# Kernel tuning notes

Hardware: AMD Instinct MI355X
Metric: run time of the kernel (lower is better)

The kernel has to match this reference:

```python
import jax, jax.numpy as jnp
import numpy as np

B, CH, XL, YL = 512, 1, 64, 64
H = 64                       # num_heads
D = CH * XL * YL             # 4096
F = D // H                   # feature_dim = 64 (== H, required by the mask multiply)


def setup_inputs() -> dict:
    key = jax.random.key(0)
    k1, k2, k3, k4, k5 = jax.random.split(key, 5)
    scale = 1.0 / np.sqrt(D)  # roughly kaiming-ish init for square linears
    return {
        "x": jax.random.normal(k1, (B, CH, XL, YL), dtype=jnp.float32),
        "interface_map": jax.random.uniform(k2, (B, CH, XL, YL), dtype=jnp.float32),
        "Wq": jax.random.normal(k3, (D, D), dtype=jnp.float32) * scale,
        "Wk": jax.random.normal(k4, (D, D), dtype=jnp.float32) * scale,
        "Wv": jax.random.normal(k5, (D, D), dtype=jnp.float32) * scale,
    }


def reference(x, interface_map, Wq, Wk, Wv):
    b = x.shape[0]
    xf = x.reshape(b, D)
    # nn.Linear(bias=False): y = x @ W.T
    q = (xf @ Wq.T).reshape(b, H, F)
    k = (xf @ Wk.T).reshape(b, H, F)
    v = (xf @ Wv.T).reshape(b, H, F)
    inv_sqrt_f = jnp.float32(1.0 / np.sqrt(F))
    qk_t = jnp.einsum("bhf,bgf->bhg", q, k) * inv_sqrt_f           # (B, H, H)
    qk_t = qk_t * interface_map.reshape(b, H, F)                   # multiplicative mask (F == H)
    attention_weights = jax.nn.softmax(qk_t, axis=-1)
    weighted_values = jnp.einsum("bhg,bgf->bhf", attention_weights, v)  # (B, H, F)
    combined = jnp.swapaxes(weighted_values, 1, 2).reshape(b, CH, XL, YL)
    output = x * combined
    return output, attention_weights
```

## Files before the change

kernel.cpp:

```cpp
#include <hip/hip_runtime.h>
#include <cstdint>
#include <cstddef>

typedef __attribute__((ext_vector_type(8))) short short8;
typedef __attribute__((ext_vector_type(4))) float f32x4;

#define NB 512
#define DD 4096
#define NP 12288

__device__ __forceinline__ unsigned pk2(float a, float b) {
    unsigned r;
    asm("v_cvt_pk_bf16_f32 %0, %1, %2" : "=v"(r) : "v"(a), "v"(b));
    return r;
}

__device__ __forceinline__ void gload_lds16(const void* g, void* l) {
    __builtin_amdgcn_global_load_lds((const __attribute__((address_space(1))) void*)g,
                                     (__attribute__((address_space(3))) void*)l, 16, 0, 0);
}

__global__ __launch_bounds__(256) void cvt_bf16_kernel(const float* __restrict__ src,
                                                       unsigned short* __restrict__ dst,
                                                       int n8) {
    int i = blockIdx.x * 256 + threadIdx.x;
    if (i >= n8) return;
    const float4* s = (const float4*)src + (size_t)i * 2;
    float4 a = s[0], b = s[1];
    uint4 r;
    r.x = pk2(a.x, a.y);
    r.y = pk2(a.z, a.w);
    r.z = pk2(b.x, b.y);
    r.w = pk2(b.z, b.w);
    ((uint4*)dst)[i] = r;
}

template<int KS>
__global__ __launch_bounds__(256, 3) void gemm_qkv_kernel(
    const unsigned short* __restrict__ xb,
    const float* __restrict__ w0, const float* __restrict__ w1, const float* __restrict__ w2,
    float* __restrict__ part)
{
    constexpr int KLEN = DD / KS;
    constexpr int NIT = KLEN / 32;
    constexpr int NWG = 96 * 4 * KS;
    constexpr int CPX = NWG / 8;

    const int bid = blockIdx.x;
    const int orig = (bid & 7) * CPX + (bid >> 3);
    const int nt = orig / (4 * KS);
    const int rest = orig - nt * (4 * KS);
    const int mt = rest / KS;
    const int kz = rest - mt * KS;

    const float* W = (nt < 32) ? w0 : ((nt < 64) ? w1 : w2);
    const int ntl = nt & 31;
    const float* Wbase = W + (size_t)(ntl * 128) * DD + kz * KLEN;
    const unsigned short* Abase = xb + (size_t)(mt * 128) * DD + kz * KLEN;
    float* C = part + (size_t)kz * NB * NP;

    __shared__ unsigned short As[4][128 * 32];
    __shared__ unsigned short Bs[2][128 * 32];

    const int t = threadIdx.x;
    const int l = t & 63;
    const int wv = t >> 6;
    const int wr = wv >> 1, wc = wv & 1;

    f32x4 acc[4][4];
    #pragma unroll
    for (int i = 0; i < 4; ++i)
        #pragma unroll
        for (int j = 0; j < 4; ++j)
            acc[i][j] = (f32x4){0.f, 0.f, 0.f, 0.f};

    const int arow0 = (t >> 2);
    const int acol  = (((t & 3) ^ ((t >> 3) & 3)) * 8);

    const int brow0 = t >> 3;
    const int bc8   = t & 7;
    const float* wsrc = Wbase + (size_t)brow0 * DD + bc8 * 4;
    char* bwp[4];
    #pragma unroll
    for (int p = 0; p < 4; ++p) {
        int r = p * 32 + brow0;
        bwp[p] = (char*)(&Bs[0][0]) + r * 64 + (((bc8 >> 1) ^ ((r >> 1) & 3)) * 16) + (bc8 & 1) * 8;
    }
    const int cx = ((l >> 4) ^ ((l >> 1) & 3));

    float4 bregA[4], bregB[4];

    #define LOADB(br, kt)  { _Pragma("unroll") for (int p = 0; p < 4; ++p) \
                               br[p] = *(const float4*)(wsrc + (size_t)(p * 32) * DD + (kt) * 32); }
    #define STAGEA(kt, buf) { _Pragma("unroll") for (int i = 0; i < 2; ++i) \
                               gload_lds16(Abase + (size_t)(i * 64 + arow0) * DD + (kt) * 32 + acol, \
                                           (char*)(&As[buf][0]) + i * 4096 + wv * 1024); }
    #define WRITEB(br, buf) { _Pragma("unroll") for (int p = 0; p < 4; ++p) { \
                                uint2 q; \
                                q.x = pk2(br[p].x, br[p].y); \
                                q.y = pk2(br[p].z, br[p].w); \
                                *(uint2*)(bwp[p] + (buf) * 8192) = q; } }
    #define BAR() { asm volatile("s_waitcnt lgkmcnt(0)" ::: "memory"); \
                    __builtin_amdgcn_s_barrier(); }

    STAGEA(0, 0);
    LOADB(bregA, 0);
    STAGEA(1, 1);
    WRITEB(bregA, 0);
    LOADB(bregB, 1);
    BAR();

    #define ITER(kt, ac, ap, bc, bn, bwr, bld) { \
        if ((kt) + 2 < NIT) { STAGEA((kt) + 2, ap); LOADB(bld, (kt) + 2); } \
        short8 af[4], bfr[4]; \
        _Pragma("unroll") for (int fi = 0; fi < 4; ++fi) { \
            int row = wr * 64 + fi * 16 + (l & 15); \
            af[fi] = *(const short8*)((const char*)(&As[ac][0]) + row * 64 + cx * 16); \
        } \
        _Pragma("unroll") for (int fj = 0; fj < 4; ++fj) { \
            int row = wc * 64 + fj * 16 + (l & 15); \
            bfr[fj] = *(const short8*)((const char*)(&Bs[bc][0]) + row * 64 + cx * 16); \
        } \
        _Pragma("unroll") for (int fi = 0; fi < 4; ++fi) \
            _Pragma("unroll") for (int fj = 0; fj < 4; ++fj) \
                acc[fi][fj] = __builtin_amdgcn_mfma_f32_16x16x32_bf16(af[fi], bfr[fj], acc[fi][fj], 0, 0, 0); \
        if ((kt) + 1 < NIT) WRITEB(bwr, bn); \
        BAR(); \
    }

    for (int kt = 0; kt < NIT; kt += 4) {
        ITER(kt + 0, 0, 2, 0, 1, bregB, bregA);
        ITER(kt + 1, 1, 3, 1, 0, bregA, bregB);
        ITER(kt + 2, 2, 0, 0, 1, bregB, bregA);
        ITER(kt + 3, 3, 1, 1, 0, bregA, bregB);
    }
    #undef ITER
    #undef LOADB
    #undef STAGEA
    #undef WRITEB
    #undef BAR

    #pragma unroll
    for (int fi = 0; fi < 4; ++fi) {
        int rbase = mt * 128 + wr * 64 + fi * 16 + (l >> 4) * 4;
        #pragma unroll
        for (int fj = 0; fj < 4; ++fj) {
            int col = nt * 128 + wc * 64 + fj * 16 + (l & 15);
            #pragma unroll
            for (int r = 0; r < 4; ++r)
                C[(size_t)(rbase + r) * NP + col] = acc[fi][fj][r];
        }
    }
}

template<int KS>
__global__ __launch_bounds__(256) void attn_kernel(
    const float* __restrict__ part,
    const float* __restrict__ x,
    const float* __restrict__ imap,
    float* __restrict__ dout)
{
    const int b = blockIdx.x;
    const int t = threadIdx.x;
    const int l = t & 63;
    const int wv = t >> 6;

    __shared__ float sq[64 * 68];
    __shared__ float sk[64 * 68];
    __shared__ float sv[64 * 68];

    const float* base0 = part + (size_t)b * NP;
    const float* base1 = part + (size_t)NB * NP + (size_t)b * NP;

    #pragma unroll
    for (int i = 0; i < 4; ++i) {
        int f4 = i * 256 + t;
        int r = f4 >> 4, c = (f4 & 15) * 4;
        float4 q4 = *(const float4*)(base0 + (size_t)f4 * 4);
        float4 k4 = *(const float4*)(base0 + DD + (size_t)f4 * 4);
        float4 v4 = *(const float4*)(base0 + 2 * DD + (size_t)f4 * 4);
        if (KS == 2) {
            float4 a4 = *(const float4*)(base1 + (size_t)f4 * 4);
            float4 b4 = *(const float4*)(base1 + DD + (size_t)f4 * 4);
            float4 c4 = *(const float4*)(base1 + 2 * DD + (size_t)f4 * 4);
            q4.x += a4.x; q4.y += a4.y; q4.z += a4.z; q4.w += a4.w;
            k4.x += b4.x; k4.y += b4.y; k4.z += b4.z; k4.w += b4.w;
            v4.x += c4.x; v4.y += c4.y; v4.z += c4.z; v4.w += c4.w;
        }
        *(float4*)(&sq[r * 68 + c]) = q4;
        *(float4*)(&sk[r * 68 + c]) = k4;
        *(float4*)(&sv[r * 68 + c]) = v4;
    }
    __syncthreads();

    float accs[16];
    #pragma unroll
    for (int i = 0; i < 16; ++i) accs[i] = 0.f;
    #pragma unroll 4
    for (int f4 = 0; f4 < 16; ++f4) {
        float4 kvv = *(const float4*)(&sk[l * 68 + f4 * 4]);
        #pragma unroll
        for (int i = 0; i < 16; ++i) {
            int h = i * 4 + wv;
            float4 qv = *(const float4*)(&sq[h * 68 + f4 * 4]);
            accs[i] = fmaf(qv.x, kvv.x, fmaf(qv.y, kvv.y, fmaf(qv.z, kvv.z, fmaf(qv.w, kvv.w, accs[i]))));
        }
    }
    __syncthreads();
    #pragma unroll
    for (int i = 0; i < 16; ++i) {
        int h = i * 4 + wv;
        float m = imap[(size_t)b * DD + h * 64 + l];
        sk[h * 65 + l] = accs[i] * 0.125f * m;
    }
    __syncthreads();

    {
        int h = t >> 2, j = t & 3;
        float e[16];
        float mx = -3.0e38f;
        #pragma unroll
        for (int q2 = 0; q2 < 16; ++q2) {
            e[q2] = sk[h * 65 + j * 16 + q2];
            mx = fmaxf(mx, e[q2]);
        }
        mx = fmaxf(mx, __shfl_xor(mx, 1));
        mx = fmaxf(mx, __shfl_xor(mx, 2));
        float s = 0.f;
        #pragma unroll
        for (int q2 = 0; q2 < 16; ++q2) { e[q2] = __expf(e[q2] - mx); s += e[q2]; }
        s += __shfl_xor(s, 1);
        s += __shfl_xor(s, 2);
        float invs = 1.0f / s;
        float* aw = dout + (size_t)NB * DD + (size_t)b * DD + h * 64 + j * 16;
        #pragma unroll
        for (int q2 = 0; q2 < 16; q2 += 4) {
            float4 w4 = {e[q2] * invs, e[q2 + 1] * invs, e[q2 + 2] * invs, e[q2 + 3] * invs};
            *(float4*)(aw + q2) = w4;
            sk[h * 65 + j * 16 + q2 + 0] = w4.x;
            sk[h * 65 + j * 16 + q2 + 1] = w4.y;
            sk[h * 65 + j * 16 + q2 + 2] = w4.z;
            sk[h * 65 + j * 16 + q2 + 3] = w4.w;
        }
    }
    __syncthreads();

    float pacc[16];
    #pragma unroll
    for (int i = 0; i < 16; ++i) pacc[i] = 0.f;
    #pragma unroll 4
    for (int g = 0; g < 64; ++g) {
        float p = sk[l * 65 + g];
        const float4* vr = (const float4*)(&sv[g * 68 + wv * 16]);
        float4 v0 = vr[0], v1 = vr[1], v2 = vr[2], v3 = vr[3];
        pacc[0]  = fmaf(p, v0.x, pacc[0]);
        pacc[1]  = fmaf(p, v0.y, pacc[1]);
        pacc[2]  = fmaf(p, v0.z, pacc[2]);
        pacc[3]  = fmaf(p, v0.w, pacc[3]);
        pacc[4]  = fmaf(p, v1.x, pacc[4]);
        pacc[5]  = fmaf(p, v1.y, pacc[5]);
        pacc[6]  = fmaf(p, v1.z, pacc[6]);
        pacc[7]  = fmaf(p, v1.w, pacc[7]);
        pacc[8]  = fmaf(p, v2.x, pacc[8]);
        pacc[9]  = fmaf(p, v2.y, pacc[9]);
        pacc[10] = fmaf(p, v2.z, pacc[10]);
        pacc[11] = fmaf(p, v2.w, pacc[11]);
        pacc[12] = fmaf(p, v3.x, pacc[12]);
        pacc[13] = fmaf(p, v3.y, pacc[13]);
        pacc[14] = fmaf(p, v3.z, pacc[14]);
        pacc[15] = fmaf(p, v3.w, pacc[15]);
    }
    const size_t ob = (size_t)b * DD + (size_t)(wv * 16) * 64 + l;
    #pragma unroll
    for (int ii = 0; ii < 16; ++ii) {
        size_t o = ob + (size_t)ii * 64;
        dout[o] = x[o] * pacc[ii];
    }
}

extern "C" void kernel_launch(void* const* d_in, const int* in_sizes, int n_in,
                              void* d_out, int out_size, void* d_ws, size_t ws_size,
                              hipStream_t stream) {
    const float* x  = (const float*)d_in[0];
    const float* im = (const float*)d_in[1];
    const float* Wq = (const float*)d_in[2];
    const float* Wk = (const float*)d_in[3];
    const float* Wv = (const float*)d_in[4];
    float* out = (float*)d_out;

    unsigned short* xb = (unsigned short*)d_ws;
    float* part = (float*)((char*)d_ws + (size_t)NB * DD * 2);

    const size_t need2 = (size_t)NB * DD * 2 + 2ull * NB * NP * 4;
    const int KS = (ws_size >= need2) ? 2 : 1;

    cvt_bf16_kernel<<<dim3((NB * DD / 8 + 255) / 256), dim3(256), 0, stream>>>(x, xb, NB * DD / 8);

    if (KS == 2) {
        gemm_qkv_kernel<2><<<dim3(96 * 4 * 2), dim3(256), 0, stream>>>(xb, Wq, Wk, Wv, part);
        attn_kernel<2><<<dim3(NB), dim3(256), 0, stream>>>(part, x, im, out);
    } else {
        gemm_qkv_kernel<1><<<dim3(96 * 4 * 1), dim3(256), 0, stream>>>(xb, Wq, Wk, Wv, part);
        attn_kernel<1><<<dim3(NB), dim3(256), 0, stream>>>(part, x, im, out);
    }
}
```

Before: 129.1 us.

## Deepen QKV GEMM prefetch pipeline to three stages with MFMA priority boost

The QKV projection GEMM now prefetches A tiles and B register tiles three iterations ahead instead of two. It rotates three B register sets and unrolls by 12 so buffer indices stay compile-time constants. MFMA blocks are wrapped in s_setprio to favour the compute wave, and the main loop barriers only wait on LDS counters, with a full vmcnt wait kept for the tail iterations. The aim is to hide more global load latency, at the cost of more registers, which could cut occupancy under launch_bounds(256,3), and a fragile loop-trip computation.

```diff
diff --git a/kernel.cpp b/kernel.cpp
--- a/kernel.cpp
+++ b/kernel.cpp
@@ -43,6 +43,7 @@
 {
     constexpr int KLEN = DD / KS;
     constexpr int NIT = KLEN / 32;
+    constexpr int KMAIN = ((NIT - 4) / 12) * 12;
     constexpr int NWG = 96 * 4 * KS;
     constexpr int CPX = NWG / 8;
 
@@ -88,7 +89,7 @@
     }
     const int cx = ((l >> 4) ^ ((l >> 1) & 3));
 
-    float4 bregA[4], bregB[4];
+    float4 b0[4], b1[4], b2[4];
 
     #define LOADB(br, kt)  { _Pragma("unroll") for (int p = 0; p < 4; ++p) \
                                br[p] = *(const float4*)(wsrc + (size_t)(p * 32) * DD + (kt) * 32); }
@@ -100,45 +101,82 @@
                                 q.x = pk2(br[p].x, br[p].y); \
                                 q.y = pk2(br[p].z, br[p].w); \
                                 *(uint2*)(bwp[p] + (buf) * 8192) = q; } }
-    #define BAR() { asm volatile("s_waitcnt lgkmcnt(0)" ::: "memory"); \
-                    __builtin_amdgcn_s_barrier(); }
-
-    STAGEA(0, 0);
-    LOADB(bregA, 0);
-    STAGEA(1, 1);
-    WRITEB(bregA, 0);
-    LOADB(bregB, 1);
-    BAR();
-
-    #define ITER(kt, ac, ap, bc, bn, bwr, bld) { \
-        if ((kt) + 2 < NIT) { STAGEA((kt) + 2, ap); LOADB(bld, (kt) + 2); } \
+    #define BARL() { asm volatile("s_waitcnt lgkmcnt(0)" ::: "memory"); \
+                     __builtin_amdgcn_s_barrier(); }
+    #define BARF() { asm volatile("s_waitcnt vmcnt(0) lgkmcnt(0)" ::: "memory"); \
+                     __builtin_amdgcn_s_barrier(); }
+
+    #define COMPUTE(abuf, bbuf) { \
         short8 af[4], bfr[4]; \
         _Pragma("unroll") for (int fi = 0; fi < 4; ++fi) { \
             int row = wr * 64 + fi * 16 + (l & 15); \
-            af[fi] = *(const short8*)((const char*)(&As[ac][0]) + row * 64 + cx * 16); \
+            af[fi] = *(const short8*)((const char*)(&As[abuf][0]) + row * 64 + cx * 16); \
         } \
         _Pragma("unroll") for (int fj = 0; fj < 4; ++fj) { \
             int row = wc * 64 + fj * 16 + (l & 15); \
-            bfr[fj] = *(const short8*)((const char*)(&Bs[bc][0]) + row * 64 + cx * 16); \
+            bfr[fj] = *(const short8*)((const char*)(&Bs[bbuf][0]) + row * 64 + cx * 16); \
         } \
+        __builtin_amdgcn_s_setprio(1); \
         _Pragma("unroll") for (int fi = 0; fi < 4; ++fi) \
             _Pragma("unroll") for (int fj = 0; fj < 4; ++fj) \
                 acc[fi][fj] = __builtin_amdgcn_mfma_f32_16x16x32_bf16(af[fi], bfr[fj], acc[fi][fj], 0, 0, 0); \
-        if ((kt) + 1 < NIT) WRITEB(bwr, bn); \
-        BAR(); \
-    }
-
-    for (int kt = 0; kt < NIT; kt += 4) {
-        ITER(kt + 0, 0, 2, 0, 1, bregB, bregA);
-        ITER(kt + 1, 1, 3, 1, 0, bregA, bregB);
-        ITER(kt + 2, 2, 0, 0, 1, bregB, bregA);
-        ITER(kt + 3, 3, 1, 1, 0, bregA, bregB);
-    }
-    #undef ITER
+        __builtin_amdgcn_s_setprio(0); \
+    }
+
+    #define ITER_M(kt, s, bl, bw) { \
+        STAGEA((kt) + 3, ((s) + 3) & 3); \
+        LOADB(bl, (kt) + 3); \
+        COMPUTE((s) & 3, (s) & 1); \
+        WRITEB(bw, ((s) + 1) & 1); \
+        BARL(); }
+
+    #define ITER_T(kt, s, bl, bw) { \
+        if ((kt) < NIT) { \
+            if ((kt) + 3 < NIT) { STAGEA((kt) + 3, ((s) + 3) & 3); LOADB(bl, (kt) + 3); } \
+            COMPUTE((s) & 3, (s) & 1); \
+            if ((kt) + 1 < NIT) WRITEB(bw, ((s) + 1) & 1); \
+            BARF(); } }
+
+    STAGEA(0, 0);
+    STAGEA(1, 1);
+    STAGEA(2, 2);
+    LOADB(b0, 0);
+    LOADB(b1, 1);
+    LOADB(b2, 2);
+    WRITEB(b0, 0);
+    BARL();
+
+    for (int kt0 = 0; kt0 < KMAIN; kt0 += 12) {
+        ITER_M(kt0 + 0,  0,  b0, b1);
+        ITER_M(kt0 + 1,  1,  b1, b2);
+        ITER_M(kt0 + 2,  2,  b2, b0);
+        ITER_M(kt0 + 3,  3,  b0, b1);
+        ITER_M(kt0 + 4,  4,  b1, b2);
+        ITER_M(kt0 + 5,  5,  b2, b0);
+        ITER_M(kt0 + 6,  6,  b0, b1);
+        ITER_M(kt0 + 7,  7,  b1, b2);
+        ITER_M(kt0 + 8,  8,  b2, b0);
+        ITER_M(kt0 + 9,  9,  b0, b1);
+        ITER_M(kt0 + 10, 10, b1, b2);
+        ITER_M(kt0 + 11, 11, b2, b0);
+    }
+    ITER_T(KMAIN + 0, 0, b0, b1);
+    ITER_T(KMAIN + 1, 1, b1, b2);
+    ITER_T(KMAIN + 2, 2, b2, b0);
+    ITER_T(KMAIN + 3, 3, b0, b1);
+    ITER_T(KMAIN + 4, 4, b1, b2);
+    ITER_T(KMAIN + 5, 5, b2, b0);
+    ITER_T(KMAIN + 6, 6, b0, b1);
+    ITER_T(KMAIN + 7, 7, b1, b2);
+
+    #undef ITER_M
+    #undef ITER_T
+    #undef COMPUTE
     #undef LOADB
     #undef STAGEA
     #undef WRITEB
-    #undef BAR
+    #undef BARL
+    #undef BARF
 
     #pragma unroll
     for (int fi = 0; fi < 4; ++fi) {
```

After: 206.9 us. +60.3%, slower.
